# Performance work log

Measured on AMD Instinct MI355X. Metric: run time of the kernel, lower is better.

The kernel has to match this reference:

```python
import math
import jax, jax.numpy as jnp
import numpy as np

C, H, W, N = 128, 64, 64, 32


def setup_inputs() -> dict:
    key = jax.random.key(0)
    k = jax.random.split(key, 6)
    std = 0.02
    return {
        "x": jax.random.normal(k[0], (N, C, H, W), dtype=jnp.float32),
        # p_3: 1x1 conv, weight [out=C, in=3C]
        "w3": jax.random.normal(k[1], (C, 3 * C), dtype=jnp.float32) * std,
        "p5_w": jax.random.normal(k[2], (1, 1, H, W), dtype=jnp.float32) * std,
        # p_6: conv (3,1), dilation (3,1), weight [O=C, I=C, 3, 1]
        "w6": jax.random.normal(k[3], (C, C, 3, 1), dtype=jnp.float32) * std,
        "p8_w": jax.random.normal(k[4], (1, C, 1, 1), dtype=jnp.float32) * std,
        "p12_w": jax.random.normal(k[5], (1, 1, 3, H, 1), dtype=jnp.float32) * std,
    }


def reference(x, w3, p5_w, w6, p8_w, p12_w):
    n, c, h, w = x.shape
    # F.unfold(x, (1,3), dilation=(1,2), padding=(0,2)) -> taps at w-2, w, w+2 (zero padded)
    xp = jnp.pad(x, ((0, 0), (0, 0), (0, 0), (2, 2)))
    t1 = jnp.stack([xp[..., 0:w], xp[..., 2:w + 2], xp[..., 4:w + 4]], axis=2)  # [n,c,3,h,w]
    t2 = t1.max(axis=2)                                                          # [n,c,h,w]
    # p_3: 1x1 conv over 3c channels
    t3 = jnp.einsum('nkhw,ok->nohw', t1.reshape(n, c * 3, h, w), w3)            # [n,c,h,w]
    t4 = jnp.maximum(t3[:, :, None], t1)                                         # [n,c,3,h,w]
    t5 = p5_w * t2
    # p_6: (3,1) conv, dilation (3,1), padding (3,0) -> same spatial size
    t6 = jax.lax.conv_general_dilated(
        t5, w6, window_strides=(1, 1), padding=((3, 3), (0, 0)),
        rhs_dilation=(3, 1), dimension_numbers=('NCHW', 'OIHW', 'NCHW'))         # [n,c,h,w]
    t7 = jnp.maximum(x, t6)
    t8 = p8_w * t7
    # bmm: [n,c,hw] x [n,hw,3c] -> [n,c,3c]
    t9 = jnp.einsum('ncp,nkp->nck', t8.reshape(n, c, h * w),
                    t1.reshape(n, c * 3, h * w)) / math.sqrt(h * w)
    t10 = t7[:, :, None] + t4                                                    # [n,c,3,h,w]
    t11 = jnp.maximum(t6[:, :, None], t10)                                       # [n,c,3,h,w]
    t12 = p12_w * t11
    # bmm: [n,hw,3c] x [n,3c,c] -> [n,hw,c]
    t13 = jnp.einsum('nkp,nck->npc', t12.reshape(n, c * 3, h * w), t9) / math.sqrt(c * 3)
    return t13.reshape(n, h, w, c).transpose(0, 3, 1, 2)                         # [n,c,h,w]
```

## Files before the change

kernel.cpp:

```cpp
#include <hip/hip_runtime.h>

#define C_   128
#define P_   4096
#define K3   384
#define CP   (C_*P_)
#define NB_  32

typedef __attribute__((ext_vector_type(8))) short short8;
typedef __attribute__((ext_vector_type(4))) short short4v;
typedef __attribute__((ext_vector_type(4))) float f32x4;

__device__ __forceinline__ short f2bf(float f) {
  union { float f; unsigned u; } v; v.f = f;
  unsigned r = v.u + 0x7fffu + ((v.u >> 16) & 1u);
  return (short)(r >> 16);
}
__device__ __forceinline__ float bf2f(short b) {
  union { unsigned u; float f; } v; v.u = ((unsigned)(unsigned short)b) << 16;
  return v.f;
}
__device__ __forceinline__ void gl_lds16(const void* g, void* l) {
  __builtin_amdgcn_global_load_lds(
      (const __attribute__((address_space(1))) unsigned int*)g,
      (__attribute__((address_space(3))) unsigned int*)l, 16, 0, 0);
}

__global__ __launch_bounds__(256) void prep_kernel(const float* __restrict__ w3,
                                                   const float* __restrict__ w6,
                                                   short* __restrict__ w3p,
                                                   short* __restrict__ w6p) {
  int idx = blockIdx.x * 256 + threadIdx.x;
  int m = idx / K3, kp = idx - m * K3;
  int j = kp >> 7, c = kp & 127;
  w3p[idx] = f2bf(w3[m * K3 + c * 3 + j]);
  w6p[idx] = f2bf(w6[m * K3 + c * 3 + j]);
}

__global__ __launch_bounds__(256) void xk_kernel(const float* __restrict__ x,
                                                 short* __restrict__ xb,
                                                 short* __restrict__ xT) {
  int b = blockIdx.x;
  int pt = b & 63, ct = (b >> 6) & 1, n = b >> 7;
  int p0 = pt * 64, c0 = ct * 64;
  const float* xn = x + (size_t)n * CP;
  short* xbn = xb + (size_t)n * CP;
  short* xTn = xT + (size_t)n * CP;
  __shared__ short Ls[64][68];
  int tid = threadIdx.x;
#pragma unroll
  for (int it = 0; it < 4; ++it) {
    int fid = tid + it * 256;
    int i = fid >> 4, j4 = fid & 15;
    f32x4 v = *(const f32x4*)(xn + (c0 + i) * P_ + p0 + j4 * 4);
    short4v s;
#pragma unroll
    for (int r = 0; r < 4; ++r) s[r] = f2bf(v[r]);
    *(short4v*)(xbn + (c0 + i) * P_ + p0 + j4 * 4) = s;
    *(short4v*)(&Ls[i][j4 * 4]) = s;
  }
  __syncthreads();
#pragma unroll
  for (int it = 0; it < 4; ++it) {
    int oid = tid + it * 256;
    int pr = oid >> 4, cg = oid & 15, cb = cg * 4;
    short4v a;
#pragma unroll
    for (int r = 0; r < 4; ++r) a[r] = Ls[cb + r][pr];
    *(short4v*)(xTn + (p0 + pr) * C_ + c0 + cb) = a;
  }
}

__global__ __launch_bounds__(256, 4) void g12_kernel(const short* __restrict__ w3p,
                                                     const short* __restrict__ w6p,
                                                     const float* __restrict__ p5,
                                                     const short* __restrict__ xT,
                                                     short* __restrict__ t3T,
                                                     short* __restrict__ t6T,
                                                     short* __restrict__ t7T) {
  int blk = blockIdx.x;
  int role = blk & 1;
  int b = blk >> 1;
  int n = b >> 5, pt = b & 31, p0 = pt * 128;
  int tid = threadIdx.x, lane = tid & 63, wv = tid >> 6;
  int wm = (wv & 1) * 64, wp = (wv >> 1) * 64;
  const short* Ap = role ? w3p : w6p;
  const short* xTn = xT + (size_t)n * CP;
  __shared__ __align__(16) short As[2][4][128][8];
  __shared__ __align__(16) short Bs[2][4][128][8];
  f32x4 acc[4][4] = {};
  short8 bm[2], bl[2], br[2];
  float bp5[2];

  auto stageA = [&](int ks, int bf) {
    int k0 = (ks % 3) * 128 + (ks / 3) * 32;
#pragma unroll
    for (int it = 0; it < 2; ++it) {
      int slot = tid + it * 256;
      int q = slot >> 7, m = slot & 127;
      gl_lds16(Ap + m * K3 + k0 + q * 8, &As[bf][q][m][0]);
    }
  };
  auto loadB = [&](int ks) {
    int jr = ks % 3;
#pragma unroll
    for (int it = 0; it < 2; ++it) {
      int slot = tid + it * 256;
      int q = slot & 3, pc = slot >> 2;
      int p = p0 + pc;
      int c0k = (ks / 3) * 32 + q * 8;
      if (role) {
        int d = 2 * (jr - 1);
        int prc = min(max(p + d, 0), P_ - 1);
        bm[it] = *(const short8*)(xTn + (size_t)prc * C_ + c0k);
      } else {
        int pr = p + 192 * (jr - 1);
        int prc = min(max(pr, 0), P_ - 1);
        int w2 = prc & 63;
        const short* rb = xTn + (size_t)prc * C_ + c0k;
        short8 zero = {};
        bm[it] = *(const short8*)rb;
        bl[it] = (w2 >= 2) ? *(const short8*)(rb - 2 * C_) : zero;
        br[it] = (w2 < 62) ? *(const short8*)(rb + 2 * C_) : zero;
        bp5[it] = p5[prc];
      }
    }
  };
  auto writeB = [&](int ks, int bf) {
    int jr = ks % 3;
#pragma unroll
    for (int it = 0; it < 2; ++it) {
      int slot = tid + it * 256;
      int q = slot & 3, pc = slot >> 2;
      int p = p0 + pc;
      short8 zero = {};
      short8 v;
      if (role) {
        int d = 2 * (jr - 1);
        int wd = (p & 63) + d;
        v = bm[it];
        if (!(wd >= 0 && wd < 64)) v = zero;
      } else {
        int pr = p + 192 * (jr - 1);
        bool rv = (pr >= 0 && pr < P_);
#pragma unroll
        for (int jj = 0; jj < 8; ++jj)
          v[jj] = f2bf(bp5[it] * fmaxf(fmaxf(bf2f(bl[it][jj]), bf2f(bm[it][jj])), bf2f(br[it][jj])));
        if (!rv) v = zero;
      }
      *(short8*)(&Bs[bf][q][pc][0]) = v;
    }
  };

  stageA(0, 0);
  loadB(0);
  writeB(0, 0);
  __syncthreads();
#pragma unroll 2
  for (int ks = 0; ks < 12; ++ks) {
    int cur = ks & 1, nxt = cur ^ 1;
    if (ks < 11) { stageA(ks + 1, nxt); loadB(ks + 1); }
    int row = lane & 15, q = lane >> 4;
    short8 a[4], bb[4];
#pragma unroll
    for (int im = 0; im < 4; ++im) a[im] = *(const short8*)(&As[cur][q][wm + im * 16 + row][0]);
#pragma unroll
    for (int ip = 0; ip < 4; ++ip) bb[ip] = *(const short8*)(&Bs[cur][q][wp + ip * 16 + row][0]);
#pragma unroll
    for (int im = 0; im < 4; ++im)
#pragma unroll
      for (int ip = 0; ip < 4; ++ip)
        acc[im][ip] = __builtin_amdgcn_mfma_f32_16x16x32_bf16(a[im], bb[ip], acc[im][ip], 0, 0, 0);
    if (ks < 11) writeB(ks + 1, nxt);
    __syncthreads();
  }
  int col = lane & 15, rq = lane >> 4;
  if (role) {
    short* t3Tn = t3T + (size_t)n * CP;
#pragma unroll
    for (int im = 0; im < 4; ++im)
#pragma unroll
      for (int ip = 0; ip < 4; ++ip) {
        int m0 = wm + im * 16 + rq * 4;
        int p = p0 + wp + ip * 16 + col;
        short4v s;
#pragma unroll
        for (int r = 0; r < 4; ++r) s[r] = f2bf(acc[im][ip][r]);
        *(short4v*)(t3Tn + (size_t)p * C_ + m0) = s;
      }
  } else {
    short* t6Tn = t6T + (size_t)n * CP;
    short* t7Tn = t7T + (size_t)n * CP;
#pragma unroll
    for (int im = 0; im < 4; ++im)
#pragma unroll
      for (int ip = 0; ip < 4; ++ip) {
        int m0 = wm + im * 16 + rq * 4;
        int p = p0 + wp + ip * 16 + col;
        short4v ax = *(const short4v*)(xTn + (size_t)p * C_ + m0);
        short4v s6, s7;
#pragma unroll
        for (int r = 0; r < 4; ++r) {
          float t6v = acc[im][ip][r];
          float t7v = fmaxf(bf2f(ax[r]), t6v);
          s6[r] = f2bf(t6v);
          s7[r] = f2bf(t7v);
        }
        *(short4v*)(t6Tn + (size_t)p * C_ + m0) = s6;
        *(short4v*)(t7Tn + (size_t)p * C_ + m0) = s7;
      }
  }
}

__global__ __launch_bounds__(256, 4) void g3_kernel(const short* __restrict__ xb,
                                                    const short* __restrict__ t7T,
                                                    float* __restrict__ t9) {
  int blk = blockIdx.x;
  int nb = blk % 3;
  int tmp = blk / 3;
  int n = tmp & 31, sk = tmp >> 5;
  int d = 2 * (nb - 1);
  int tid = threadIdx.x, lane = tid & 63, wv = tid >> 6;
  int wm = (wv & 1) * 64, wp = (wv >> 1) * 64;
  const short* xbn = xb + (size_t)n * CP;
  const short* t7n = t7T + (size_t)n * CP;
  __shared__ __align__(16) short As[2][4][128][8];
  __shared__ __align__(16) short Bs[2][4][128][8];
  f32x4 acc[4][4] = {};
  short8 av[2], bv[2];

  auto loadAB = [&](int ks) {
    int pp0 = sk * 512 + ks * 32;
#pragma unroll
    for (int it = 0; it < 2; ++it) {
      int slot = tid + it * 256;
      int q = slot >> 7, rr = slot & 127;
      int pb = pp0 + q * 8;
      const int* src = (const int*)(xbn + rr * P_ + pb + d);
      union { int i[4]; short8 s; } u;
#pragma unroll
      for (int t = 0; t < 4; ++t) u.i[t] = src[t];
      av[it] = u.s;
      const short* bp = t7n + (size_t)pb * C_ + rr;
      short8 w;
#pragma unroll
      for (int j = 0; j < 8; ++j) w[j] = bp[j * C_];
      bv[it] = w;
    }
  };
  auto writeAB = [&](int ks, int bf) {
    int pp0 = sk * 512 + ks * 32;
#pragma unroll
    for (int it = 0; it < 2; ++it) {
      int slot = tid + it * 256;
      int q = slot >> 7, rr = slot & 127;
      int pb = pp0 + q * 8;
      short8 v = av[it];
      int w0 = pb & 63;
      if (nb == 0) { if (w0 == 0) { v[0] = 0; v[1] = 0; } }
      else if (nb == 2) { if (w0 == 56) { v[6] = 0; v[7] = 0; } }
      *(short8*)(&As[bf][q][rr][0]) = v;
      *(short8*)(&Bs[bf][q][rr][0]) = bv[it];
    }
  };

  loadAB(0);
  writeAB(0, 0);
  __syncthreads();
#pragma unroll 2
  for (int ks = 0; ks < 16; ++ks) {
    int cur = ks & 1, nxt = cur ^ 1;
    if (ks < 15) loadAB(ks + 1);
    int row = lane & 15, q = lane >> 4;
    short8 a[4], bb[4];
#pragma unroll
    for (int im = 0; im < 4; ++im) a[im] = *(const short8*)(&As[cur][q][wm + im * 16 + row][0]);
#pragma unroll
    for (int ip = 0; ip < 4; ++ip) bb[ip] = *(const short8*)(&Bs[cur][q][wp + ip * 16 + row][0]);
#pragma unroll
    for (int im = 0; im < 4; ++im)
#pragma unroll
      for (int ip = 0; ip < 4; ++ip)
        acc[im][ip] = __builtin_amdgcn_mfma_f32_16x16x32_bf16(a[im], bb[ip], acc[im][ip], 0, 0, 0);
    if (ks < 15) writeAB(ks + 1, nxt);
    __syncthreads();
  }
  int col = lane & 15, rq = lane >> 4;
  float* t9n = t9 + (size_t)n * (K3 * C_);
#pragma unroll
  for (int im = 0; im < 4; ++im)
#pragma unroll
    for (int ip = 0; ip < 4; ++ip)
#pragma unroll
      for (int r = 0; r < 4; ++r) {
        int kp = nb * 128 + wm + im * 16 + rq * 4 + r;
        int c = wp + ip * 16 + col;
        atomicAdd(&t9n[(size_t)kp * C_ + c], acc[im][ip][r]);
      }
}

__global__ __launch_bounds__(256) void t9s_kernel(const float* __restrict__ t9,
                                                  const float* __restrict__ p8,
                                                  short* __restrict__ t9b) {
  int b = blockIdx.x;
  int n = b / 6, kt = b - n * 6;
  int k0 = kt * 64;
  const float INV = 1.0f / (64.0f * 19.5959179423f);
  const float* t9n = t9 + (size_t)n * (K3 * C_);
  short* t9bn = t9b + (size_t)n * (C_ * K3);
  __shared__ float L[64][132];
  int tid = threadIdx.x;
#pragma unroll
  for (int it = 0; it < 8; ++it) {
    int s = tid + it * 256;
    int k = s >> 5, c4 = s & 31;
    f32x4 v = *(const f32x4*)(t9n + (size_t)(k0 + k) * C_ + c4 * 4);
    *(f32x4*)(&L[k][c4 * 4]) = v;
  }
  __syncthreads();
#pragma unroll
  for (int it = 0; it < 2; ++it) {
    int s = tid + it * 256;
    int c = s >> 2, kg = s & 3;
    float sc = p8[c] * INV;
    short8 o0, o1;
#pragma unroll
    for (int j = 0; j < 8; ++j) o0[j] = f2bf(L[kg * 16 + j][c] * sc);
#pragma unroll
    for (int j = 0; j < 8; ++j) o1[j] = f2bf(L[kg * 16 + 8 + j][c] * sc);
    short* op = t9bn + (size_t)c * K3 + k0 + kg * 16;
    *(short8*)(op) = o0;
    *(short8*)(op + 8) = o1;
  }
}

__global__ __launch_bounds__(256) void t12k_kernel(const float* __restrict__ p12,
                                                   const short* __restrict__ xT,
                                                   short* __restrict__ t3T,
                                                   short* __restrict__ t6T,
                                                   short* __restrict__ t7T) {
  int idx = blockIdx.x * 256 + threadIdx.x;
  int cg = idx & 15;
  int p  = (idx >> 4) & 4095;
  int n  = idx >> 16;
  size_t base = (size_t)n * CP + (size_t)p * C_ + cg * 8;
  short8 a3 = *(const short8*)(t3T + base);
  short8 a6 = *(const short8*)(t6T + base);
  short8 a7 = *(const short8*)(t7T + base);
  const short* xn = xT + (size_t)n * CP;
  int c0 = cg * 8;
  int h = p >> 6, w = p & 63;
  short8 outv[3];
#pragma unroll
  for (int j = 0; j < 3; ++j) {
    int d = 2 * (j - 1);
    int wd = w + d;
    bool valid = (wd >= 0 && wd < 64);
    int pr = min(max(p + d, 0), P_ - 1);
    short8 ax = *(const short8*)(xn + (size_t)pr * C_ + c0);
    short8 zero = {};
    if (!valid) ax = zero;
    float s12 = p12[j * 64 + h];
    short8 v;
#pragma unroll
    for (int jj = 0; jj < 8; ++jj) {
      float t11 = fmaxf(bf2f(a6[jj]), bf2f(a7[jj]) + fmaxf(bf2f(a3[jj]), bf2f(ax[jj])));
      v[jj] = f2bf(s12 * t11);
    }
    outv[j] = v;
  }
  *(short8*)(t3T + base) = outv[0];
  *(short8*)(t6T + base) = outv[1];
  *(short8*)(t7T + base) = outv[2];
}

__global__ __launch_bounds__(256, 4) void g4_kernel(const short* __restrict__ t9b,
                                                    const short* __restrict__ t12,
                                                    float* __restrict__ out) {
  int b = blockIdx.x;
  int n = b >> 5, pt = b & 31, p0 = pt * 128;
  int tid = threadIdx.x, lane = tid & 63, wv = tid >> 6;
  int wm = (wv & 1) * 64, wp = (wv >> 1) * 64;
  const short* t9n = t9b + (size_t)n * (K3 * C_);
  const size_t SL = (size_t)NB_ * CP;
  __shared__ __align__(16) short As[2][4][128][8];
  __shared__ __align__(16) short Bs[2][4][128][8];
  f32x4 acc[4][4] = {};

  auto stageA = [&](int ks, int bf) {
    int k0 = (ks % 3) * 128 + (ks / 3) * 32;
#pragma unroll
    for (int it = 0; it < 2; ++it) {
      int slot = tid + it * 256;
      int q = slot >> 7, m = slot & 127;
      gl_lds16(t9n + (size_t)m * K3 + k0 + q * 8, &As[bf][q][m][0]);
    }
  };
  auto stageB = [&](int ks, int bf) {
    int j = ks % 3, cb = ks / 3;
    const short* src = t12 + (size_t)j * SL + (size_t)n * CP;
#pragma unroll
    for (int it = 0; it < 2; ++it) {
      int slot = tid + it * 256;
      int q = slot >> 7, pc = slot & 127;
      gl_lds16(src + (size_t)(p0 + pc) * C_ + cb * 32 + q * 8, &Bs[bf][q][pc][0]);
    }
  };

  stageA(0, 0);
  stageB(0, 0);
  __syncthreads();
#pragma unroll 2
  for (int ks = 0; ks < 12; ++ks) {
    int cur = ks & 1, nxt = cur ^ 1;
    if (ks < 11) { stageA(ks + 1, nxt); stageB(ks + 1, nxt); }
    int row = lane & 15, q = lane >> 4;
    short8 a[4], bb[4];
#pragma unroll
    for (int im = 0; im < 4; ++im) a[im] = *(const short8*)(&As[cur][q][wm + im * 16 + row][0]);
#pragma unroll
    for (int ip = 0; ip < 4; ++ip) bb[ip] = *(const short8*)(&Bs[cur][q][wp + ip * 16 + row][0]);
#pragma unroll
    for (int im = 0; im < 4; ++im)
#pragma unroll
      for (int ip = 0; ip < 4; ++ip)
        acc[im][ip] = __builtin_amdgcn_mfma_f32_16x16x32_bf16(a[im], bb[ip], acc[im][ip], 0, 0, 0);
    __syncthreads();
  }
  int col = lane & 15, rq = lane >> 4;
#pragma unroll
  for (int im = 0; im < 4; ++im)
#pragma unroll
    for (int ip = 0; ip < 4; ++ip)
#pragma unroll
      for (int r = 0; r < 4; ++r) {
        int m = wm + im * 16 + rq * 4 + r;
        int p = p0 + wp + ip * 16 + col;
        out[(size_t)n * CP + m * P_ + p] = acc[im][ip][r];
      }
}

extern "C" void kernel_launch(void* const* d_in, const int* in_sizes, int n_in,
                              void* d_out, int out_size, void* d_ws, size_t ws_size,
                              hipStream_t stream) {
  const float* x   = (const float*)d_in[0];
  const float* w3  = (const float*)d_in[1];
  const float* p5  = (const float*)d_in[2];
  const float* w6  = (const float*)d_in[3];
  const float* p8  = (const float*)d_in[4];
  const float* p12 = (const float*)d_in[5];
  float* out = (float*)d_out;

  char* ws = (char*)d_ws;
  const size_t RB = (size_t)NB_ * CP * 2;
  size_t off = 256;
  short* xb  = (short*)(ws + off); off += RB;
  short* xT  = (short*)(ws + off); off += RB;
  short* t3T = (short*)(ws + off); off += RB;
  short* t6T = (short*)(ws + off); off += RB;
  short* t7T = (short*)(ws + off); off += RB;
  float* t9  = (float*)(ws + off); off += (size_t)NB_ * K3 * C_ * 4;
  short* w3p = (short*)(ws + off); off += 49152 * 2;
  short* w6p = (short*)(ws + off); off += 49152 * 2;
  short* t9b = xb;

  prep_kernel<<<192, 256, 0, stream>>>(w3, w6, w3p, w6p);
  xk_kernel<<<4096, 256, 0, stream>>>(x, xb, xT);
  g12_kernel<<<2048, 256, 0, stream>>>(w3p, w6p, p5, xT, t3T, t6T, t7T);
  hipMemsetAsync(t9, 0, (size_t)NB_ * K3 * C_ * sizeof(float), stream);
  g3_kernel<<<768, 256, 0, stream>>>(xb, t7T, t9);
  t9s_kernel<<<192, 256, 0, stream>>>(t9, p8, t9b);
  t12k_kernel<<<8192, 256, 0, stream>>>(p12, xT, t3T, t6T, t7T);
  g4_kernel<<<1024, 256, 0, stream>>>(t9b, t3T, out);
}
```

Before: 399.8 us.

## Precompute zero-padded t5 buffer in xk and stream it to LDS asynchronously

The t5 = p5*max(x[w-2],x[w],x[w+2]) computation moves out of the g12 conv GEMM into the transpose kernel. Its output goes into a bf16 buffer with 192 rows of zero padding on each side, stored in the output buffer, which is free until the last kernel. The conv role of g12 can then fill its B tile with direct global-to-LDS loads instead of three gathered reads, elementwise math and an LDS write per step. In exchange it adds a memset and one extra write and read of a roughly 37MB intermediate.

```diff
diff --git a/kernel.cpp b/kernel.cpp
--- a/kernel.cpp
+++ b/kernel.cpp
@@ -5,6 +5,7 @@
 #define K3   384
 #define CP   (C_*P_)
 #define NB_  32
+#define PR_  4480
 
 typedef __attribute__((ext_vector_type(8))) short short8;
 typedef __attribute__((ext_vector_type(4))) short short4v;
@@ -37,14 +38,17 @@
 }
 
 __global__ __launch_bounds__(256) void xk_kernel(const float* __restrict__ x,
+                                                 const float* __restrict__ p5,
                                                  short* __restrict__ xb,
-                                                 short* __restrict__ xT) {
+                                                 short* __restrict__ xT,
+                                                 short* __restrict__ t5p) {
   int b = blockIdx.x;
   int pt = b & 63, ct = (b >> 6) & 1, n = b >> 7;
   int p0 = pt * 64, c0 = ct * 64;
   const float* xn = x + (size_t)n * CP;
   short* xbn = xb + (size_t)n * CP;
   short* xTn = xT + (size_t)n * CP;
+  short* t5n = t5p + (size_t)n * PR_ * C_;
   __shared__ short Ls[64][68];
   int tid = threadIdx.x;
 #pragma unroll
@@ -63,16 +67,24 @@
   for (int it = 0; it < 4; ++it) {
     int oid = tid + it * 256;
     int pr = oid >> 4, cg = oid & 15, cb = cg * 4;
-    short4v a;
-#pragma unroll
-    for (int r = 0; r < 4; ++r) a[r] = Ls[cb + r][pr];
+    float p5v = p5[p0 + pr];
+    short4v a, t5v;
+#pragma unroll
+    for (int r = 0; r < 4; ++r) {
+      a[r] = Ls[cb + r][pr];
+      float m = bf2f(a[r]);
+      float l = (pr >= 2) ? bf2f(Ls[cb + r][pr - 2]) : 0.0f;
+      float rr = (pr < 62) ? bf2f(Ls[cb + r][pr + 2]) : 0.0f;
+      t5v[r] = f2bf(p5v * fmaxf(fmaxf(l, m), rr));
+    }
     *(short4v*)(xTn + (p0 + pr) * C_ + c0 + cb) = a;
+    *(short4v*)(t5n + (size_t)(192 + p0 + pr) * C_ + c0 + cb) = t5v;
   }
 }
 
 __global__ __launch_bounds__(256, 4) void g12_kernel(const short* __restrict__ w3p,
                                                      const short* __restrict__ w6p,
-                                                     const float* __restrict__ p5,
+                                                     const short* __restrict__ t5p,
                                                      const short* __restrict__ xT,
                                                      short* __restrict__ t3T,
                                                      short* __restrict__ t6T,
@@ -85,11 +97,11 @@
   int wm = (wv & 1) * 64, wp = (wv >> 1) * 64;
   const short* Ap = role ? w3p : w6p;
   const short* xTn = xT + (size_t)n * CP;
+  const short* t5n = t5p + (size_t)n * PR_ * C_;
   __shared__ __align__(16) short As[2][4][128][8];
   __shared__ __align__(16) short Bs[2][4][128][8];
   f32x4 acc[4][4] = {};
-  short8 bm[2], bl[2], br[2];
-  float bp5[2];
+  short8 bm[2];
 
   auto stageA = [&](int ks, int bf) {
     int k0 = (ks % 3) * 128 + (ks / 3) * 32;
@@ -100,7 +112,17 @@
       gl_lds16(Ap + m * K3 + k0 + q * 8, &As[bf][q][m][0]);
     }
   };
-  auto loadB = [&](int ks) {
+  auto stageB0 = [&](int ks, int bf) {
+    int jr = ks % 3, cb = ks / 3;
+    const short* src = t5n + (size_t)(jr * 192 + p0) * C_ + cb * 32;
+#pragma unroll
+    for (int it = 0; it < 2; ++it) {
+      int slot = tid + it * 256;
+      int q = slot >> 7, pc = slot & 127;
+      gl_lds16(src + (size_t)pc * C_ + q * 8, &Bs[bf][q][pc][0]);
+    }
+  };
+  auto loadB1 = [&](int ks) {
     int jr = ks % 3;
 #pragma unroll
     for (int it = 0; it < 2; ++it) {
@@ -108,57 +130,37 @@
       int q = slot & 3, pc = slot >> 2;
       int p = p0 + pc;
       int c0k = (ks / 3) * 32 + q * 8;
-      if (role) {
-        int d = 2 * (jr - 1);
-        int prc = min(max(p + d, 0), P_ - 1);
-        bm[it] = *(const short8*)(xTn + (size_t)prc * C_ + c0k);
-      } else {
-        int pr = p + 192 * (jr - 1);
-        int prc = min(max(pr, 0), P_ - 1);
-        int w2 = prc & 63;
-        const short* rb = xTn + (size_t)prc * C_ + c0k;
-        short8 zero = {};
-        bm[it] = *(const short8*)rb;
-        bl[it] = (w2 >= 2) ? *(const short8*)(rb - 2 * C_) : zero;
-        br[it] = (w2 < 62) ? *(const short8*)(rb + 2 * C_) : zero;
-        bp5[it] = p5[prc];
-      }
-    }
-  };
-  auto writeB = [&](int ks, int bf) {
+      int d = 2 * (jr - 1);
+      int prc = min(max(p + d, 0), P_ - 1);
+      bm[it] = *(const short8*)(xTn + (size_t)prc * C_ + c0k);
+    }
+  };
+  auto writeB1 = [&](int ks, int bf) {
     int jr = ks % 3;
 #pragma unroll
     for (int it = 0; it < 2; ++it) {
       int slot = tid + it * 256;
       int q = slot & 3, pc = slot >> 2;
       int p = p0 + pc;
+      int d = 2 * (jr - 1);
+      int wd = (p & 63) + d;
       short8 zero = {};
-      short8 v;
-      if (role) {
-        int d = 2 * (jr - 1);
-        int wd = (p & 63) + d;
-        v = bm[it];
-        if (!(wd >= 0 && wd < 64)) v = zero;
-      } else {
-        int pr = p + 192 * (jr - 1);
-        bool rv = (pr >= 0 && pr < P_);
-#pragma unroll
-        for (int jj = 0; jj < 8; ++jj)
-          v[jj] = f2bf(bp5[it] * fmaxf(fmaxf(bf2f(bl[it][jj]), bf2f(bm[it][jj])), bf2f(br[it][jj])));
-        if (!rv) v = zero;
-      }
+      short8 v = bm[it];
+      if (!(wd >= 0 && wd < 64)) v = zero;
       *(short8*)(&Bs[bf][q][pc][0]) = v;
     }
   };
 
   stageA(0, 0);
-  loadB(0);
-  writeB(0, 0);
+  if (role) { loadB1(0); writeB1(0, 0); } else stageB0(0, 0);
   __syncthreads();
 #pragma unroll 2
   for (int ks = 0; ks < 12; ++ks) {
     int cur = ks & 1, nxt = cur ^ 1;
-    if (ks < 11) { stageA(ks + 1, nxt); loadB(ks + 1); }
+    if (ks < 11) {
+      stageA(ks + 1, nxt);
+      if (role) loadB1(ks + 1); else stageB0(ks + 1, nxt);
+    }
     int row = lane & 15, q = lane >> 4;
     short8 a[4], bb[4];
 #pragma unroll
@@ -170,7 +172,7 @@
 #pragma unroll
       for (int ip = 0; ip < 4; ++ip)
         acc[im][ip] = __builtin_amdgcn_mfma_f32_16x16x32_bf16(a[im], bb[ip], acc[im][ip], 0, 0, 0);
-    if (ks < 11) writeB(ks + 1, nxt);
+    if (ks < 11 && role) writeB1(ks + 1, nxt);
     __syncthreads();
   }
   int col = lane & 15, rq = lane >> 4;
@@ -462,10 +464,12 @@
   short* w3p = (short*)(ws + off); off += 49152 * 2;
   short* w6p = (short*)(ws + off); off += 49152 * 2;
   short* t9b = xb;
+  short* t5p = (short*)out;
 
   prep_kernel<<<192, 256, 0, stream>>>(w3, w6, w3p, w6p);
-  xk_kernel<<<4096, 256, 0, stream>>>(x, xb, xT);
-  g12_kernel<<<2048, 256, 0, stream>>>(w3p, w6p, p5, xT, t3T, t6T, t7T);
+  hipMemsetAsync(t5p, 0, (size_t)NB_ * PR_ * C_ * 2, stream);
+  xk_kernel<<<4096, 256, 0, stream>>>(x, p5, xb, xT, t5p);
+  g12_kernel<<<2048, 256, 0, stream>>>(w3p, w6p, t5p, xT, t3T, t6T, t7T);
   hipMemsetAsync(t9, 0, (size_t)NB_ * K3 * C_ * sizeof(float), stream);
   g3_kernel<<<768, 256, 0, stream>>>(xb, t7T, t9);
   t9s_kernel<<<192, 256, 0, stream>>>(t9, p8, t9b);
```

Measured after the change: 415.3 us. 3.9% more time.
